# Optimization experiments

Hardware: AMD Instinct MI355X
Metric: run time of the kernel (lower is better)

Reference implementation:

```python
import jax, jax.numpy as jnp
import numpy as np

T, N, D, E, O = 2, 4096, 1024, 8, 1024

def setup_inputs() -> dict:
    key = jax.random.key(0)
    k1, k2, k3 = jax.random.split(key, 3)
    x = jax.random.normal(k1, (T, N, D), dtype=jnp.float32)
    Wg = jax.random.normal(k2, (T, D, E), dtype=jnp.float32) * (1.0 / np.sqrt(D))
    We = jax.random.normal(k3, (E, D, O), dtype=jnp.float32) * (1.0 / np.sqrt(D))
    return {"x": x, "Wg": Wg, "We": We, "k": 2}


def reference(x, Wg, We, k):
    # Per-task gating logits: [T, N, E]
    logits = jnp.einsum('tnd,tde->tne', x, Wg)
    # Top-k mask per token (scatter 1.0 at top-k indices)
    _, topk_idx = jax.lax.top_k(logits, k)                      # [T, N, k]
    mask = jax.nn.one_hot(topk_idx, E, dtype=logits.dtype).sum(-2)  # [T, N, E]
    masked = mask * logits
    gates = masked / (masked.sum(-1, keepdims=True) + 1e-9)     # [T, N, E]
    # Dense expert outputs (each expert is Linear(D, O)): [T, N, E, O]
    eout = jnp.einsum('tnd,edo->tneo', x, We)
    # Weighted combine over selected experts
    out = jnp.einsum('tne,tneo->tno', gates, eout)              # [T, N, O]
    return out
```

## Files before the change

kernel.cpp:

```cpp
#include <hip/hip_runtime.h>
#include <hip/hip_bf16.h>
#include <stdint.h>

#define T_ 2
#define N_ 4096
#define D_ 1024
#define E_ 8
#define O_ 1024

#define BM 128
#define BN 128
#define BK 32

typedef __attribute__((ext_vector_type(8))) short short8;
typedef __attribute__((ext_vector_type(4))) float f32x4;

#define AS1 __attribute__((address_space(1)))
#define AS3 __attribute__((address_space(3)))

__device__ inline void gld16(const unsigned short* g, unsigned short* l) {
    __builtin_amdgcn_global_load_lds((const AS1 unsigned int*)g,
                                     (AS3 unsigned int*)l, 16, 0, 0);
}

__device__ inline unsigned short f2bf(float f) {
    union { float f; unsigned u; } v; v.f = f;
    unsigned r = v.u + 0x7fff + ((v.u >> 16) & 1);
    return (unsigned short)(r >> 16);
}

__global__ __launch_bounds__(256) void gate_kernel(
    const float* __restrict__ x, const float* __restrict__ Wg,
    unsigned short* __restrict__ xb,
    int* __restrict__ route, float2* __restrict__ gpair)
{
    __shared__ __align__(16) float WgT[E_][D_];

    int tid = threadIdx.x;
    int wave = tid >> 6, lane = tid & 63;
    int token0 = blockIdx.x * 8;
    int t = token0 >> 12;
    const float* wgb = Wg + (size_t)t * D_ * E_;

#pragma unroll
    for (int r = 0; r < 8; ++r) {
        int f = r * 1024 + tid * 4;
        float4 v = *(const float4*)(wgb + f);
        WgT[f & 7][f >> 3]             = v.x;
        WgT[(f + 1) & 7][(f + 1) >> 3] = v.y;
        WgT[(f + 2) & 7][(f + 2) >> 3] = v.z;
        WgT[(f + 3) & 7][(f + 3) >> 3] = v.w;
    }
    __syncthreads();

#pragma unroll
    for (int tl = 0; tl < 2; ++tl) {
        int token = token0 + wave * 2 + tl;
        const float* xrow = x + (size_t)token * D_;

        float4 xv[4];
#pragma unroll
        for (int c = 0; c < 4; ++c)
            xv[c] = *(const float4*)(xrow + c * 256 + lane * 4);

        float acc[E_] = {0.f, 0.f, 0.f, 0.f, 0.f, 0.f, 0.f, 0.f};
#pragma unroll
        for (int c = 0; c < 4; ++c) {
            int d0 = c * 256 + lane * 4;
            unsigned lo = f2bf(xv[c].x) | ((unsigned)f2bf(xv[c].y) << 16);
            unsigned hi = f2bf(xv[c].z) | ((unsigned)f2bf(xv[c].w) << 16);
            *(uint2*)(&xb[(size_t)token * D_ + d0]) = make_uint2(lo, hi);
#pragma unroll
            for (int e = 0; e < E_; ++e) {
                float4 w = *(const float4*)(&WgT[e][d0]);
                acc[e] += xv[c].x * w.x + xv[c].y * w.y + xv[c].z * w.z + xv[c].w * w.w;
            }
        }
#pragma unroll
        for (int off = 1; off < 64; off <<= 1) {
#pragma unroll
            for (int e = 0; e < E_; ++e) acc[e] += __shfl_xor(acc[e], off, 64);
        }

        if (lane == 0) {
            float best = acc[0]; int bi = 0;
#pragma unroll
            for (int e = 1; e < E_; ++e) if (acc[e] > best) { best = acc[e]; bi = e; }
            float sec = -INFINITY; int si = 0;
#pragma unroll
            for (int e = 0; e < E_; ++e) if (e != bi && acc[e] > sec) { sec = acc[e]; si = e; }
            float s = best + sec + 1e-9f;
            route[token] = bi | (si << 8);
            gpair[token] = make_float2(best / s, sec / s);
        }
    }
}

__global__ __launch_bounds__(1024) void build_lists(
    const int* __restrict__ route, const float2* __restrict__ gpair,
    int* __restrict__ toklist, float* __restrict__ gatelist,
    int* __restrict__ counts)
{
    int g = blockIdx.x;
    int t = g >> 3, e = g & 7;
    int tid = threadIdx.x;
    int wave = tid >> 6, lane = tid & 63;

    __shared__ int waveSum[16];
    __shared__ int base;
    if (tid == 0) base = 0;

    for (int c = 0; c < N_; c += 1024) {
        int n = c + tid;
        int r = route[t * N_ + n];
        int e0 = r & 255, e1 = (r >> 8) & 255;
        bool sel = (e0 == e) || (e1 == e);
        unsigned long long b = __ballot(sel);
        int pre  = __popcll(b & ((1ull << lane) - 1ull));
        if (lane == 0) waveSum[wave] = __popcll(b);
        __syncthreads();
        int woff = 0, total = 0;
#pragma unroll
        for (int w = 0; w < 16; ++w) {
            int s = waveSum[w];
            total += s;
            woff += (w < wave) ? s : 0;
        }
        if (sel) {
            int p = base + woff + pre;
            int slot = (e0 == e) ? 0 : 1;
            toklist[g * N_ + p] = n | (slot << 16);
            float2 gp = gpair[t * N_ + n];
            gatelist[g * N_ + p] = (e0 == e) ? gp.x : gp.y;
        }
        __syncthreads();
        if (tid == 0) base += total;
    }
    __syncthreads();
    if (tid == 0) counts[g] = base;
}

__global__ __launch_bounds__(256) void pack_kernel(
    const float* __restrict__ We, unsigned short* __restrict__ Wbp)
{
    __shared__ __align__(16) unsigned short P[64 * 136];

    int b = blockIdx.x;
    int e  = b >> 7;
    int oy = (b & 127) >> 3;
    int dz = b & 7;
    int o0 = oy * 64, d0 = dz * 128;
    int tid = threadIdx.x;

#pragma unroll
    for (int r = 0; r < 32; ++r) {
        int lin = r * 256 + tid;
        int dd = lin >> 6, oo = lin & 63;
        P[oo * 136 + dd] = f2bf(We[((size_t)(e * D_ + d0 + dd)) * O_ + o0 + oo]);
    }
    __syncthreads();

#pragma unroll
    for (int w = 0; w < 4; ++w) {
        int ci = w * 256 + tid;
        int oo = ci >> 4, dc = ci & 15;
        uint4 v = *(const uint4*)&P[oo * 136 + dc * 8];
        int o = o0 + oo;
        int ot = o >> 7, nn = o & 127;
        unsigned short* dst =
            Wbp + ((size_t)((e * 8 + ot) * 128 + nn)) * D_ + d0 + dc * 8;
        *(uint4*)dst = v;
    }
}

__global__ __launch_bounds__(256) void moe_gemm(
    const unsigned short* __restrict__ xb,
    const unsigned short* __restrict__ Wbp,
    const int* __restrict__ toklist, const float* __restrict__ gatelist,
    const int* __restrict__ counts, float* __restrict__ out)
{
    int lin = blockIdx.x;
    int mt  = lin >> 7;
    int u   = lin & 127;
    int xcd = u & 7;
    int v   = u >> 3;
    int g   = 2 * xcd + (v >> 3);
    int ot  = v & 7;
    int t   = g >> 3;

    int cnt = counts[g];
    int m0 = mt * BM;
    if (m0 >= cnt) return;

    __shared__ __align__(16) unsigned short As[2][BM * BK];
    __shared__ __align__(16) unsigned short Bs[2][BN * BK];
    __shared__ int   tokS[BM];
    __shared__ float gateS[BM];

    int tid = threadIdx.x;
    if (tid < BM) {
        int r = m0 + tid;
        tokS[tid]  = (r < cnt) ? toklist[g * N_ + r]  : -1;
        gateS[tid] = (r < cnt) ? gatelist[g * N_ + r] : 0.f;
    }
    __syncthreads();

    int wave = tid >> 6, lane = tid & 63;
    int lr = lane >> 2;
    int sg = (lane & 3) ^ ((lane >> 3) & 3);
    int c0 = wave * 2, c1 = c0 + 1;
    int ar0 = c0 * 16 + lr, ar1 = c1 * 16 + lr;
    int tok0 = max(tokS[ar0], 0) & 0xFFFF;
    int tok1 = max(tokS[ar1], 0) & 0xFFFF;
    const unsigned short* ag0 = xb + ((size_t)(t * N_ + tok0)) * D_ + sg * 8;
    const unsigned short* ag1 = xb + ((size_t)(t * N_ + tok1)) * D_ + sg * 8;
    const unsigned short* wb  = Wbp + ((size_t)((g & 7) * 8 + ot) * 128) * D_;
    const unsigned short* bg0 = wb + (size_t)ar0 * D_ + sg * 8;
    const unsigned short* bg1 = wb + (size_t)ar1 * D_ + sg * 8;

    int fr = lane & 15, q = lane >> 4;
    int wm = (wave & 1) * 64, wn = (wave >> 1) * 64;
    int fp = (q ^ ((fr >> 1) & 3)) * 8;

    f32x4 acc[4][4];
#pragma unroll
    for (int mi = 0; mi < 4; ++mi)
#pragma unroll
        for (int ni = 0; ni < 4; ++ni) acc[mi][ni] = (f32x4){0.f, 0.f, 0.f, 0.f};

    gld16(ag0, &As[0][c0 * 512]);
    gld16(ag1, &As[0][c1 * 512]);
    gld16(bg0, &Bs[0][c0 * 512]);
    gld16(bg1, &Bs[0][c1 * 512]);

#define KSTEP(CUR, NXT, IT)                                                    \
    {                                                                          \
        __syncthreads();   \
        int k1 = ((IT) + 1) * BK;                                              \
        if (k1 < D_) {                                                         \
            gld16(ag0 + k1, &As[NXT][c0 * 512]);                               \
            gld16(ag1 + k1, &As[NXT][c1 * 512]);                               \
            gld16(bg0 + k1, &Bs[NXT][c0 * 512]);                               \
            gld16(bg1 + k1, &Bs[NXT][c1 * 512]);                               \
        }                                                                      \
        short8 af[4], bf[4];                                                   \
        _Pragma("unroll") for (int mi = 0; mi < 4; ++mi)                       \
            af[mi] = *(const short8*)(&As[CUR][(wm + mi * 16 + fr) * BK + fp]);\
        _Pragma("unroll") for (int ni = 0; ni < 4; ++ni)                       \
            bf[ni] = *(const short8*)(&Bs[CUR][(wn + ni * 16 + fr) * BK + fp]);\
        _Pragma("unroll") for (int mi = 0; mi < 4; ++mi)                       \
            _Pragma("unroll") for (int ni = 0; ni < 4; ++ni)                   \
                acc[mi][ni] = __builtin_amdgcn_mfma_f32_16x16x32_bf16(         \
                    af[mi], bf[ni], acc[mi][ni], 0, 0, 0);                     \
    }

    for (int it = 0; it < D_ / BK; it += 2) {
        KSTEP(0, 1, it)
        KSTEP(1, 0, it + 1)
    }
#undef KSTEP

    float* outb = out + (size_t)t * N_ * O_;
    int ncol = ot * 128 + wn + fr;
#pragma unroll
    for (int mi = 0; mi < 4; ++mi) {
#pragma unroll
        for (int r = 0; r < 4; ++r) {
            int ml = wm + mi * 16 + q * 4 + r;
            int ent = tokS[ml];
            if (ent >= 0) {
                int tok  = ent & 0xFFFF;
                int slot = ent >> 16;
                float gate = gateS[ml];
#pragma unroll
                for (int ni = 0; ni < 4; ++ni) {
                    unsigned short* p =
                        (unsigned short*)(outb + (size_t)tok * O_ + ncol + ni * 16);
                    p[slot] = f2bf(gate * acc[mi][ni][r]);
                }
            }
        }
    }
}

__global__ __launch_bounds__(256) void combine_kernel(float* __restrict__ out)
{
    size_t i = ((size_t)blockIdx.x * 256 + threadIdx.x) * 4;
    unsigned* po = (unsigned*)out;
    uint4 v = *(uint4*)(po + i);
    float4 r;
    union { unsigned u; float f; } a, b;
#define CMB(comp, src) a.u = (src) << 16; b.u = (src) & 0xFFFF0000u; comp = a.f + b.f
    CMB(r.x, v.x); CMB(r.y, v.y); CMB(r.z, v.z); CMB(r.w, v.w);
#undef CMB
    *(float4*)(out + i) = r;
}

extern "C" void kernel_launch(void* const* d_in, const int* in_sizes, int n_in,
                              void* d_out, int out_size, void* d_ws, size_t ws_size,
                              hipStream_t stream)
{
    const float* x  = (const float*)d_in[0];
    const float* Wg = (const float*)d_in[1];
    const float* We = (const float*)d_in[2];
    float* out = (float*)d_out;

    char* ws = (char*)d_ws;
    unsigned short* xb   = (unsigned short*)(ws);
    unsigned short* Wbp  = (unsigned short*)(ws + 16777216);
    int*   toklist       = (int*)  (ws + 33554432);
    float* gatelist      = (float*)(ws + 33816576);
    int*   counts        = (int*)  (ws + 34078720);
    int*   route         = (int*)  (ws + 34078976);
    float2* gpair        = (float2*)(ws + 34111744);

    gate_kernel<<<(T_ * N_) / 8, 256, 0, stream>>>(x, Wg, xb, route, gpair);
    build_lists<<<T_ * E_, 1024, 0, stream>>>(route, gpair, toklist, gatelist, counts);
    pack_kernel<<<E_ * (O_ / 64) * (D_ / 128), 256, 0, stream>>>(We, Wbp);
    moe_gemm<<<(N_ / BM) * 8 * (T_ * E_), 256, 0, stream>>>(
        xb, Wbp, toklist, gatelist, counts, out);
    combine_kernel<<<((size_t)T_ * N_ * O_) / (256 * 4), 256, 0, stream>>>(out);
}
```

Measured before the change: 192.1 us.

## Triple-buffer LDS tiles with two-stage-ahead prefetch and explicit vmcnt waits

Moves the expert GEMM main loop from double to triple buffering in LDS, keeping two K-tiles of global-to-LDS loads in flight. Each step waits on a partial vmcnt instead of a full __syncthreads drain. It also raises wave priority around the MFMA block with s_setprio. The aim is to hide global load latency better, at the cost of 50% more LDS per block, which may reduce occupancy.

Measured after the change: 205.4 us. 1.07x slower.

```diff
diff --git a/kernel.cpp b/kernel.cpp
--- a/kernel.cpp
+++ b/kernel.cpp
@@ -192,8 +192,8 @@
     int m0 = mt * BM;
     if (m0 >= cnt) return;
 
-    __shared__ __align__(16) unsigned short As[2][BM * BK];
-    __shared__ __align__(16) unsigned short Bs[2][BN * BK];
+    __shared__ __align__(16) unsigned short As[3][BM * BK];
+    __shared__ __align__(16) unsigned short Bs[3][BN * BK];
     __shared__ int   tokS[BM];
     __shared__ float gateS[BM];
 
@@ -228,37 +228,46 @@
 #pragma unroll
         for (int ni = 0; ni < 4; ++ni) acc[mi][ni] = (f32x4){0.f, 0.f, 0.f, 0.f};
 
-    gld16(ag0, &As[0][c0 * 512]);
-    gld16(ag1, &As[0][c1 * 512]);
-    gld16(bg0, &Bs[0][c0 * 512]);
-    gld16(bg1, &Bs[0][c1 * 512]);
-
-#define KSTEP(CUR, NXT, IT)                                                    \
+#define STAGE(BUF, KOFF)                                                       \
     {                                                                          \
-        __syncthreads();   \
-        int k1 = ((IT) + 1) * BK;                                              \
-        if (k1 < D_) {                                                         \
-            gld16(ag0 + k1, &As[NXT][c0 * 512]);                               \
-            gld16(ag1 + k1, &As[NXT][c1 * 512]);                               \
-            gld16(bg0 + k1, &Bs[NXT][c0 * 512]);                               \
-            gld16(bg1 + k1, &Bs[NXT][c1 * 512]);                               \
-        }                                                                      \
+        gld16(ag0 + (KOFF), &As[BUF][c0 * 512]);                               \
+        gld16(ag1 + (KOFF), &As[BUF][c1 * 512]);                               \
+        gld16(bg0 + (KOFF), &Bs[BUF][c0 * 512]);                               \
+        gld16(bg1 + (KOFF), &Bs[BUF][c1 * 512]);                               \
+    }
+
+    STAGE(0, 0)
+    STAGE(1, BK)
+
+#define KSTEP(CUR, SPARE, KOFF, VM, DOSTAGE)                                   \
+    {                                                                          \
+        asm volatile("s_waitcnt vmcnt(" #VM ")" ::: "memory");                 \
+        __builtin_amdgcn_s_barrier();                                          \
+        asm volatile("" ::: "memory");             \
+        __builtin_amdgcn_sched_barrier(0);                      \
+        if (DOSTAGE) STAGE(SPARE, KOFF)                                        \
         short8 af[4], bf[4];                                                   \
         _Pragma("unroll") for (int mi = 0; mi < 4; ++mi)                       \
             af[mi] = *(const short8*)(&As[CUR][(wm + mi * 16 + fr) * BK + fp]);\
         _Pragma("unroll") for (int ni = 0; ni < 4; ++ni)                       \
             bf[ni] = *(const short8*)(&Bs[CUR][(wn + ni * 16 + fr) * BK + fp]);\
+        __builtin_amdgcn_s_setprio(1);                                         \
         _Pragma("unroll") for (int mi = 0; mi < 4; ++mi)                       \
             _Pragma("unroll") for (int ni = 0; ni < 4; ++ni)                   \
                 acc[mi][ni] = __builtin_amdgcn_mfma_f32_16x16x32_bf16(         \
                     af[mi], bf[ni], acc[mi][ni], 0, 0, 0);                     \
-    }
-
-    for (int it = 0; it < D_ / BK; it += 2) {
-        KSTEP(0, 1, it)
-        KSTEP(1, 0, it + 1)
-    }
+        __builtin_amdgcn_s_setprio(0);                                         \
+    }
+
+    for (int it = 0; it < 30; it += 3) {
+        KSTEP(0, 2, (size_t)(it + 2) * BK, 4, 1)
+        KSTEP(1, 0, (size_t)(it + 3) * BK, 4, 1)
+        KSTEP(2, 1, (size_t)(it + 4) * BK, 4, 1)
+    }
+    KSTEP(0, 2, 0, 4, 0)
+    KSTEP(1, 2, 0, 0, 0)
 #undef KSTEP
+#undef STAGE
 
     float* outb = out + (size_t)t * N_ * O_;
     int ncol = ot * 128 + wn + fr;
```

## Merge gate and weight-pack kernels; use 8 waves per block in MoE GEMM

Applied to the files above, without the earlier changes.

The gating kernel and the expert-weight pack kernel are fused into one launch, with block ranges splitting the work, so the two independent prep stages run concurrently and one launch is dropped. The grouped GEMM moves from 4 to 8 waves per 128x128 tile. Each wave now computes a 64x32 sub-tile with half the accumulators and issues one async LDS load per operand instead of two, aiming for more latency hiding and higher occupancy. The trade-off is more waves contending for the same LDS tile and barriers, and less MFMA work per wave between syncs.

Result: faster. 183.5 us (-4.4%).

```diff
diff --git a/kernel.cpp b/kernel.cpp
--- a/kernel.cpp
+++ b/kernel.cpp
@@ -29,69 +29,101 @@
     return (unsigned short)(r >> 16);
 }
 
-__global__ __launch_bounds__(256) void gate_kernel(
+__global__ __launch_bounds__(256) void prep_kernel(
     const float* __restrict__ x, const float* __restrict__ Wg,
-    unsigned short* __restrict__ xb,
+    const float* __restrict__ We,
+    unsigned short* __restrict__ xb, unsigned short* __restrict__ Wbp,
     int* __restrict__ route, float2* __restrict__ gpair)
 {
-    __shared__ __align__(16) float WgT[E_][D_];
-
+    __shared__ __align__(16) char smem[E_ * D_ * 4];
     int tid = threadIdx.x;
-    int wave = tid >> 6, lane = tid & 63;
-    int token0 = blockIdx.x * 8;
-    int t = token0 >> 12;
-    const float* wgb = Wg + (size_t)t * D_ * E_;
-
-#pragma unroll
-    for (int r = 0; r < 8; ++r) {
-        int f = r * 1024 + tid * 4;
-        float4 v = *(const float4*)(wgb + f);
-        WgT[f & 7][f >> 3]             = v.x;
-        WgT[(f + 1) & 7][(f + 1) >> 3] = v.y;
-        WgT[(f + 2) & 7][(f + 2) >> 3] = v.z;
-        WgT[(f + 3) & 7][(f + 3) >> 3] = v.w;
-    }
-    __syncthreads();
-
-#pragma unroll
-    for (int tl = 0; tl < 2; ++tl) {
-        int token = token0 + wave * 2 + tl;
-        const float* xrow = x + (size_t)token * D_;
-
-        float4 xv[4];
-#pragma unroll
-        for (int c = 0; c < 4; ++c)
-            xv[c] = *(const float4*)(xrow + c * 256 + lane * 4);
-
-        float acc[E_] = {0.f, 0.f, 0.f, 0.f, 0.f, 0.f, 0.f, 0.f};
-#pragma unroll
-        for (int c = 0; c < 4; ++c) {
-            int d0 = c * 256 + lane * 4;
-            unsigned lo = f2bf(xv[c].x) | ((unsigned)f2bf(xv[c].y) << 16);
-            unsigned hi = f2bf(xv[c].z) | ((unsigned)f2bf(xv[c].w) << 16);
-            *(uint2*)(&xb[(size_t)token * D_ + d0]) = make_uint2(lo, hi);
-#pragma unroll
-            for (int e = 0; e < E_; ++e) {
-                float4 w = *(const float4*)(&WgT[e][d0]);
-                acc[e] += xv[c].x * w.x + xv[c].y * w.y + xv[c].z * w.z + xv[c].w * w.w;
+
+    if (blockIdx.x < 1024) {
+        float (*WgT)[D_] = (float(*)[D_])smem;
+        int wave = tid >> 6, lane = tid & 63;
+        int token0 = blockIdx.x * 8;
+        int t = token0 >> 12;
+        const float* wgb = Wg + (size_t)t * D_ * E_;
+
+#pragma unroll
+        for (int r = 0; r < 8; ++r) {
+            int f = r * 1024 + tid * 4;
+            float4 v = *(const float4*)(wgb + f);
+            WgT[f & 7][f >> 3]             = v.x;
+            WgT[(f + 1) & 7][(f + 1) >> 3] = v.y;
+            WgT[(f + 2) & 7][(f + 2) >> 3] = v.z;
+            WgT[(f + 3) & 7][(f + 3) >> 3] = v.w;
+        }
+        __syncthreads();
+
+#pragma unroll
+        for (int tl = 0; tl < 2; ++tl) {
+            int token = token0 + wave * 2 + tl;
+            const float* xrow = x + (size_t)token * D_;
+
+            float4 xv[4];
+#pragma unroll
+            for (int c = 0; c < 4; ++c)
+                xv[c] = *(const float4*)(xrow + c * 256 + lane * 4);
+
+            float acc[E_] = {0.f, 0.f, 0.f, 0.f, 0.f, 0.f, 0.f, 0.f};
+#pragma unroll
+            for (int c = 0; c < 4; ++c) {
+                int d0 = c * 256 + lane * 4;
+                unsigned lo = f2bf(xv[c].x) | ((unsigned)f2bf(xv[c].y) << 16);
+                unsigned hi = f2bf(xv[c].z) | ((unsigned)f2bf(xv[c].w) << 16);
+                *(uint2*)(&xb[(size_t)token * D_ + d0]) = make_uint2(lo, hi);
+#pragma unroll
+                for (int e = 0; e < E_; ++e) {
+                    float4 w = *(const float4*)(&WgT[e][d0]);
+                    acc[e] += xv[c].x * w.x + xv[c].y * w.y + xv[c].z * w.z + xv[c].w * w.w;
+                }
             }
-        }
-#pragma unroll
-        for (int off = 1; off < 64; off <<= 1) {
-#pragma unroll
-            for (int e = 0; e < E_; ++e) acc[e] += __shfl_xor(acc[e], off, 64);
-        }
-
-        if (lane == 0) {
-            float best = acc[0]; int bi = 0;
-#pragma unroll
-            for (int e = 1; e < E_; ++e) if (acc[e] > best) { best = acc[e]; bi = e; }
-            float sec = -INFINITY; int si = 0;
-#pragma unroll
-            for (int e = 0; e < E_; ++e) if (e != bi && acc[e] > sec) { sec = acc[e]; si = e; }
-            float s = best + sec + 1e-9f;
-            route[token] = bi | (si << 8);
-            gpair[token] = make_float2(best / s, sec / s);
+#pragma unroll
+            for (int off = 1; off < 64; off <<= 1) {
+#pragma unroll
+                for (int e = 0; e < E_; ++e) acc[e] += __shfl_xor(acc[e], off, 64);
+            }
+
+            if (lane == 0) {
+                float best = acc[0]; int bi = 0;
+#pragma unroll
+                for (int e = 1; e < E_; ++e) if (acc[e] > best) { best = acc[e]; bi = e; }
+                float sec = -INFINITY; int si = 0;
+#pragma unroll
+                for (int e = 0; e < E_; ++e) if (e != bi && acc[e] > sec) { sec = acc[e]; si = e; }
+                float s = best + sec + 1e-9f;
+                route[token] = bi | (si << 8);
+                gpair[token] = make_float2(best / s, sec / s);
+            }
+        }
+    } else {
+        unsigned short* P = (unsigned short*)smem;
+
+        int b = blockIdx.x - 1024;
+        int e  = b >> 7;
+        int oy = (b & 127) >> 3;
+        int dz = b & 7;
+        int o0 = oy * 64, d0 = dz * 128;
+
+#pragma unroll
+        for (int r = 0; r < 32; ++r) {
+            int lin = r * 256 + tid;
+            int dd = lin >> 6, oo = lin & 63;
+            P[oo * 136 + dd] = f2bf(We[((size_t)(e * D_ + d0 + dd)) * O_ + o0 + oo]);
+        }
+        __syncthreads();
+
+#pragma unroll
+        for (int w = 0; w < 4; ++w) {
+            int ci = w * 256 + tid;
+            int oo = ci >> 4, dc = ci & 15;
+            uint4 v = *(const uint4*)&P[oo * 136 + dc * 8];
+            int o = o0 + oo;
+            int ot = o >> 7, nn = o & 127;
+            unsigned short* dst =
+                Wbp + ((size_t)((e * 8 + ot) * 128 + nn)) * D_ + d0 + dc * 8;
+            *(uint4*)dst = v;
         }
     }
 }
@@ -140,40 +172,7 @@
     if (tid == 0) counts[g] = base;
 }
 
-__global__ __launch_bounds__(256) void pack_kernel(
-    const float* __restrict__ We, unsigned short* __restrict__ Wbp)
-{
-    __shared__ __align__(16) unsigned short P[64 * 136];
-
-    int b = blockIdx.x;
-    int e  = b >> 7;
-    int oy = (b & 127) >> 3;
-    int dz = b & 7;
-    int o0 = oy * 64, d0 = dz * 128;
-    int tid = threadIdx.x;
-
-#pragma unroll
-    for (int r = 0; r < 32; ++r) {
-        int lin = r * 256 + tid;
-        int dd = lin >> 6, oo = lin & 63;
-        P[oo * 136 + dd] = f2bf(We[((size_t)(e * D_ + d0 + dd)) * O_ + o0 + oo]);
-    }
-    __syncthreads();
-
-#pragma unroll
-    for (int w = 0; w < 4; ++w) {
-        int ci = w * 256 + tid;
-        int oo = ci >> 4, dc = ci & 15;
-        uint4 v = *(const uint4*)&P[oo * 136 + dc * 8];
-        int o = o0 + oo;
-        int ot = o >> 7, nn = o & 127;
-        unsigned short* dst =
-            Wbp + ((size_t)((e * 8 + ot) * 128 + nn)) * D_ + d0 + dc * 8;
-        *(uint4*)dst = v;
-    }
-}
-
-__global__ __launch_bounds__(256) void moe_gemm(
+__global__ __launch_bounds__(512, 4) void moe_gemm(
     const unsigned short* __restrict__ xb,
     const unsigned short* __restrict__ Wbp,
     const int* __restrict__ toklist, const float* __restrict__ gatelist,
@@ -208,48 +207,41 @@
     int wave = tid >> 6, lane = tid & 63;
     int lr = lane >> 2;
     int sg = (lane & 3) ^ ((lane >> 3) & 3);
-    int c0 = wave * 2, c1 = c0 + 1;
-    int ar0 = c0 * 16 + lr, ar1 = c1 * 16 + lr;
-    int tok0 = max(tokS[ar0], 0) & 0xFFFF;
-    int tok1 = max(tokS[ar1], 0) & 0xFFFF;
-    const unsigned short* ag0 = xb + ((size_t)(t * N_ + tok0)) * D_ + sg * 8;
-    const unsigned short* ag1 = xb + ((size_t)(t * N_ + tok1)) * D_ + sg * 8;
-    const unsigned short* wb  = Wbp + ((size_t)((g & 7) * 8 + ot) * 128) * D_;
-    const unsigned short* bg0 = wb + (size_t)ar0 * D_ + sg * 8;
-    const unsigned short* bg1 = wb + (size_t)ar1 * D_ + sg * 8;
+    int ar = wave * 16 + lr;
+    int tok = max(tokS[ar], 0) & 0xFFFF;
+    const unsigned short* ag = xb + ((size_t)(t * N_ + tok)) * D_ + sg * 8;
+    const unsigned short* wb = Wbp + ((size_t)((g & 7) * 8 + ot) * 128) * D_;
+    const unsigned short* bg = wb + (size_t)ar * D_ + sg * 8;
 
     int fr = lane & 15, q = lane >> 4;
-    int wm = (wave & 1) * 64, wn = (wave >> 1) * 64;
+    int wm = (wave & 1) * 64;
+    int wn = (wave >> 1) * 32;
     int fp = (q ^ ((fr >> 1) & 3)) * 8;
 
-    f32x4 acc[4][4];
+    f32x4 acc[4][2];
 #pragma unroll
     for (int mi = 0; mi < 4; ++mi)
 #pragma unroll
-        for (int ni = 0; ni < 4; ++ni) acc[mi][ni] = (f32x4){0.f, 0.f, 0.f, 0.f};
-
-    gld16(ag0, &As[0][c0 * 512]);
-    gld16(ag1, &As[0][c1 * 512]);
-    gld16(bg0, &Bs[0][c0 * 512]);
-    gld16(bg1, &Bs[0][c1 * 512]);
+        for (int ni = 0; ni < 2; ++ni) acc[mi][ni] = (f32x4){0.f, 0.f, 0.f, 0.f};
+
+    gld16(ag, &As[0][wave * 512]);
+    gld16(bg, &Bs[0][wave * 512]);
 
 #define KSTEP(CUR, NXT, IT)                                                    \
     {                                                                          \
         __syncthreads();   \
         int k1 = ((IT) + 1) * BK;                                              \
         if (k1 < D_) {                                                         \
-            gld16(ag0 + k1, &As[NXT][c0 * 512]);                               \
-            gld16(ag1 + k1, &As[NXT][c1 * 512]);                               \
-            gld16(bg0 + k1, &Bs[NXT][c0 * 512]);                               \
-            gld16(bg1 + k1, &Bs[NXT][c1 * 512]);                               \
+            gld16(ag + k1, &As[NXT][wave * 512]);                              \
+            gld16(bg + k1, &Bs[NXT][wave * 512]);                              \
         }                                                                      \
-        short8 af[4], bf[4];                                                   \
+        short8 af[4], bf[2];                                                   \
         _Pragma("unroll") for (int mi = 0; mi < 4; ++mi)                       \
             af[mi] = *(const short8*)(&As[CUR][(wm + mi * 16 + fr) * BK + fp]);\
-        _Pragma("unroll") for (int ni = 0; ni < 4; ++ni)                       \
+        _Pragma("unroll") for (int ni = 0; ni < 2; ++ni)                       \
             bf[ni] = *(const short8*)(&Bs[CUR][(wn + ni * 16 + fr) * BK + fp]);\
         _Pragma("unroll") for (int mi = 0; mi < 4; ++mi)                       \
-            _Pragma("unroll") for (int ni = 0; ni < 4; ++ni)                   \
+            _Pragma("unroll") for (int ni = 0; ni < 2; ++ni)                   \
                 acc[mi][ni] = __builtin_amdgcn_mfma_f32_16x16x32_bf16(         \
                     af[mi], bf[ni], acc[mi][ni], 0, 0, 0);                     \
     }
@@ -269,13 +261,13 @@
             int ml = wm + mi * 16 + q * 4 + r;
             int ent = tokS[ml];
             if (ent >= 0) {
-                int tok  = ent & 0xFFFF;
+                int tokk = ent & 0xFFFF;
                 int slot = ent >> 16;
                 float gate = gateS[ml];
 #pragma unroll
-                for (int ni = 0; ni < 4; ++ni) {
+                for (int ni = 0; ni < 2; ++ni) {
                     unsigned short* p =
-                        (unsigned short*)(outb + (size_t)tok * O_ + ncol + ni * 16);
+                        (unsigned short*)(outb + (size_t)tokk * O_ + ncol + ni * 16);
                     p[slot] = f2bf(gate * acc[mi][ni][r]);
                 }
             }
@@ -314,10 +306,9 @@
     int*   route         = (int*)  (ws + 34078976);
     float2* gpair        = (float2*)(ws + 34111744);
 
-    gate_kernel<<<(T_ * N_) / 8, 256, 0, stream>>>(x, Wg, xb, route, gpair);
+    prep_kernel<<<2048, 256, 0, stream>>>(x, Wg, We, xb, Wbp, route, gpair);
     build_lists<<<T_ * E_, 1024, 0, stream>>>(route, gpair, toklist, gatelist, counts);
-    pack_kernel<<<E_ * (O_ / 64) * (D_ / 128), 256, 0, stream>>>(We, Wbp);
-    moe_gemm<<<(N_ / BM) * 8 * (T_ * E_), 256, 0, stream>>>(
+    moe_gemm<<<(N_ / BM) * 8 * (T_ * E_), 512, 0, stream>>>(
         xb, Wbp, toklist, gatelist, counts, out);
     combine_kernel<<<((size_t)T_ * N_ * O_) / (256 * 4), 256, 0, stream>>>(out);
 }
```
